# Performance work log

Hardware: AMD Instinct MI355X
Metric: run time of the kernel (lower is better)

The kernel has to match this reference:

```python
import jax, jax.numpy as jnp
import numpy as np

N_NODES = 50000
N_EDGES = 800000
IN_DIM = 128
OUT_DIM = 128
NUM_HEADS = 8
HEAD_DIM = OUT_DIM // NUM_HEADS
LN_EPS = 1e-5


def setup_inputs() -> dict:
    key = jax.random.key(0)
    ks = jax.random.split(key, 8)
    # xavier-uniform bounds
    def xavier(k, shape, fan_in, fan_out):
        a = float(np.sqrt(6.0 / (fan_in + fan_out)))
        return jax.random.uniform(k, shape, jnp.float32, -a, a)
    x = jax.random.normal(ks[0], (N_NODES, IN_DIM), jnp.float32)
    edge_index = jax.random.randint(ks[1], (2, N_EDGES), 0, N_NODES, jnp.int32)
    # store Linear weights as (in, out) so forward is x @ W (same math as torch x @ W.T)
    W_src = xavier(ks[2], (IN_DIM, OUT_DIM), IN_DIM, OUT_DIM)
    W_dst = xavier(ks[3], (IN_DIM, OUT_DIM), IN_DIM, OUT_DIM)
    attn = xavier(ks[4], (NUM_HEADS, HEAD_DIM), HEAD_DIM, NUM_HEADS)
    W_out = xavier(ks[5], (OUT_DIM, OUT_DIM), OUT_DIM, OUT_DIM)
    b_out = jnp.zeros((OUT_DIM,), jnp.float32)
    gamma = jnp.ones((OUT_DIM,), jnp.float32)
    beta = jnp.zeros((OUT_DIM,), jnp.float32)
    return {"x": x, "edge_index": edge_index, "W_src": W_src, "W_dst": W_dst,
            "attn": attn, "W_out": W_out, "b_out": b_out, "gamma": gamma, "beta": beta}


def reference(x, edge_index, W_src, W_dst, attn, W_out, b_out, gamma, beta):
    N = x.shape[0]
    H, D = attn.shape
    src, dst = edge_index[0], edge_index[1]
    # node transforms: (N, H, D)
    h_src = (x @ W_src).reshape(N, H, D)
    h_dst = (x @ W_dst).reshape(N, H, D)
    # per-edge GATv2 attention logits (E, H)
    h_src_e = h_src[src]                                  # (E, H, D)
    e = jax.nn.leaky_relu(h_src_e + h_dst[dst], 0.2)
    s = jnp.einsum('ehd,hd->eh', e, attn)
    # segment (scatter) softmax over incoming edges of each dst node
    m = jax.ops.segment_max(s, dst, num_segments=N)       # (N, H)
    exp = jnp.exp(s - m[dst])
    denom = jax.ops.segment_sum(exp, dst, num_segments=N)
    alpha = exp / (denom[dst] + 1e-8)                     # (E, H)
    # weighted message aggregation
    msg = (h_src_e * alpha[..., None]).reshape(-1, H * D)
    out = jax.ops.segment_sum(msg, dst, num_segments=N)   # (N, H*D)
    out = out @ W_out + b_out
    out = out + x                                          # residual (in_dim == out_dim)
    # LayerNorm
    mu = jnp.mean(out, axis=-1, keepdims=True)
    var = jnp.var(out, axis=-1, keepdims=True)
    out = (out - mu) * jax.lax.rsqrt(var + LN_EPS) * gamma + beta
    return out
```

## Files before the change

kernel.cpp:

```cpp
#include <hip/hip_runtime.h>
#include <hip/hip_bf16.h>

#define HEADS 8
#define CDIM 128
#define CAP 96
#define CHUNK 2048

typedef __attribute__((ext_vector_type(8))) short bf16x8;
typedef __attribute__((ext_vector_type(4))) float f32x4;

__device__ __forceinline__ unsigned short f2bs(float f) {
    union { __hip_bfloat16 b; unsigned short u; } c;
    c.b = __float2bfloat16(f);
    return c.u;
}

__device__ __forceinline__ float dpp_reduce8(float p) {
    p += __int_as_float(__builtin_amdgcn_update_dpp(0, __float_as_int(p), 0x141, 0xF, 0xF, true));
    p += __int_as_float(__builtin_amdgcn_update_dpp(0, __float_as_int(p), 0xB1,  0xF, 0xF, true));
    p += __int_as_float(__builtin_amdgcn_update_dpp(0, __float_as_int(p), 0x4E,  0xF, 0xF, true));
    return p;
}

__global__ __launch_bounds__(256) void prep_kernel(
        const int* __restrict__ ei,
        int* __restrict__ cnt,
        int* __restrict__ bucket,
        const float* __restrict__ Wsrc,
        const float* __restrict__ Wdst,
        const float* __restrict__ Wout,
        unsigned short* __restrict__ WT,
        unsigned short* __restrict__ WoT, int E, int nedgeblk) {
    const int b = blockIdx.x;
    if (b < nedgeblk) {
        const int shard = b & 7;
        const int base = (b >> 3) * CHUNK;
        int end = base + CHUNK; if (end > E) end = E;
        for (int e = base + (int)threadIdx.x; e < end; e += 256) {
            const int dst = ei[E + e];
            if ((dst & 7) == shard) {
                const int src = ei[e];
                const int pos = atomicAdd(&cnt[dst], 1);
                if (pos < CAP) bucket[(size_t)dst * CAP + pos] = src;
            }
        }
        return;
    }
    int i = (b - nedgeblk) * 256 + threadIdx.x;
    if (i < 16384)      { WT[i] = f2bs(Wsrc[(i & 127) * CDIM + (i >> 7)]); }
    else if (i < 32768) { int j = i - 16384; WT[16384 + j] = f2bs(Wdst[(j & 127) * CDIM + (j >> 7)]); }
    else if (i < 49152) { int j = i - 32768; WoT[j] = f2bs(Wout[(j & 127) * CDIM + (j >> 7)]); }
}

__global__ __launch_bounds__(256) void transform_mfma64(
        const float* __restrict__ x,
        const unsigned short* __restrict__ WT,
        unsigned short* __restrict__ hsrc,
        unsigned short* __restrict__ hdst, int N) {
    __shared__ unsigned short As[64][136];
    __shared__ unsigned short Bs[128][136];
    const int t = threadIdx.x;
    const int m0 = blockIdx.x * 64;
    const int half = blockIdx.y;
    for (int i = t; i < 64 * 32; i += 256) {
        const int r = i >> 5, kq = i & 31;
        const int gr = m0 + r;
        float4 v = make_float4(0.f, 0.f, 0.f, 0.f);
        if (gr < N) v = *(const float4*)(x + (size_t)gr * CDIM + kq * 4);
        uint2 pk;
        pk.x = (unsigned)f2bs(v.x) | ((unsigned)f2bs(v.y) << 16);
        pk.y = (unsigned)f2bs(v.z) | ((unsigned)f2bs(v.w) << 16);
        *(uint2*)&As[r][kq * 4] = pk;
    }
    const unsigned short* Wb = WT + (size_t)half * 16384;
    for (int i = t; i < 128 * 16; i += 256) {
        const int r = i >> 4, q = i & 15;
        *(uint4*)&Bs[r][q * 8] = *(const uint4*)(Wb + (size_t)r * CDIM + q * 8);
    }
    __syncthreads();
    const int w = t >> 6, lane = t & 63, l16 = lane & 15, quad = lane >> 4;
    const int wm = (w & 1) * 32, wn = (w >> 1) * 64;
    f32x4 acc[2][4];
#pragma unroll
    for (int mi = 0; mi < 2; mi++)
#pragma unroll
        for (int ni = 0; ni < 4; ni++) acc[mi][ni] = (f32x4){0.f, 0.f, 0.f, 0.f};
#pragma unroll
    for (int kc = 0; kc < 4; kc++) {
        const int k0 = kc * 32 + quad * 8;
        bf16x8 af[2], bf[4];
        af[0] = *(const bf16x8*)&As[wm + l16][k0];
        af[1] = *(const bf16x8*)&As[wm + 16 + l16][k0];
#pragma unroll
        for (int ni = 0; ni < 4; ni++)
            bf[ni] = *(const bf16x8*)&Bs[wn + ni * 16 + l16][k0];
#pragma unroll
        for (int mi = 0; mi < 2; mi++)
#pragma unroll
            for (int ni = 0; ni < 4; ni++)
                acc[mi][ni] = __builtin_amdgcn_mfma_f32_16x16x32_bf16(af[mi], bf[ni], acc[mi][ni], 0, 0, 0);
    }
    unsigned short* H = half ? hdst : hsrc;
#pragma unroll
    for (int mi = 0; mi < 2; mi++)
#pragma unroll
        for (int reg = 0; reg < 4; reg++) {
            const int gm = m0 + wm + mi * 16 + quad * 4 + reg;
            if (gm < N) {
#pragma unroll
                for (int ni = 0; ni < 4; ni++)
                    H[(size_t)gm * CDIM + wn + ni * 16 + l16] = f2bs(acc[mi][ni][reg]);
            }
        }
}

__global__ __launch_bounds__(256) void attn_agg5(
        const unsigned short* __restrict__ hsrc,
        const unsigned short* __restrict__ hdst,
        const float* __restrict__ attn,
        const int* __restrict__ cnt,
        const int* __restrict__ bucket,
        unsigned short* __restrict__ aggb) {
    __shared__ int src_lds[4][CAP];
    const int t = threadIdx.x;
    const int w = t >> 6, lane = t & 63;
    const int dst = blockIdx.x * 4 + w;
    int deg = cnt[dst];
    deg = deg > CAP ? CAP : deg;
    for (int j = lane; j < deg; j += 64)
        src_lds[w][j] = bucket[(size_t)dst * CAP + j];

    const unsigned hu = *(const unsigned*)(hdst + (size_t)dst * CDIM + lane * 2);
    const float hd0 = __uint_as_float(hu << 16);
    const float hd1 = __uint_as_float(hu & 0xffff0000u);
    const float2 a2 = ((const float2*)attn)[lane];
    const unsigned short* hb = hsrc + lane * 2;

    float l = 0.f, acc0 = 0.f, acc1 = 0.f;
    for (int j0 = 0; j0 < deg; j0 += 16) {
        unsigned vv[16];
#pragma unroll
        for (int p = 0; p < 16; p++) {
            const int j = j0 + p;
            vv[p] = (j < deg) ? *(const unsigned*)(hb + (size_t)src_lds[w][j] * CDIM) : 0u;
        }
#pragma unroll
        for (int p = 0; p < 16; p++) {
            const int j = j0 + p;
            if (j < deg) {
                const float v0 = __uint_as_float(vv[p] << 16);
                const float v1 = __uint_as_float(vv[p] & 0xffff0000u);
                float e0 = v0 + hd0; e0 = fmaxf(e0, 0.2f * e0);
                float e1 = v1 + hd1; e1 = fmaxf(e1, 0.2f * e1);
                const float pp = dpp_reduce8(e0 * a2.x + e1 * a2.y);
                const float wgt = __expf(pp);
                l += wgt;
                acc0 = fmaf(wgt, v0, acc0);
                acc1 = fmaf(wgt, v1, acc1);
            }
        }
    }
    const float r = 1.f / (l + 1e-8f);
    const unsigned o = (unsigned)f2bs(acc0 * r) | ((unsigned)f2bs(acc1 * r) << 16);
    *(unsigned*)(aggb + (size_t)dst * CDIM + lane * 2) = o;
}

__global__ __launch_bounds__(256) void out_mfma_ln64(
        const unsigned short* __restrict__ aggb,
        const float* __restrict__ x,
        const unsigned short* __restrict__ WoT,
        const float* __restrict__ bo,
        const float* __restrict__ gam,
        const float* __restrict__ bet,
        float* __restrict__ out, int N) {
    __shared__ unsigned short As[64][136];
    __shared__ unsigned short Bs[128][136];
    __shared__ float red1[64][2], red2[64][2];
    __shared__ float s_mu[64], s_rs[64];
    const int t = threadIdx.x;
    const int m0 = blockIdx.x * 64;
    for (int i = t; i < 64 * 16; i += 256) {
        const int r = i >> 4, q = i & 15;
        const int gr = m0 + r;
        uint4 v = make_uint4(0u, 0u, 0u, 0u);
        if (gr < N) v = *(const uint4*)(aggb + (size_t)gr * CDIM + q * 8);
        *(uint4*)&As[r][q * 8] = v;
    }
    for (int i = t; i < 128 * 16; i += 256) {
        const int r = i >> 4, q = i & 15;
        *(uint4*)&Bs[r][q * 8] = *(const uint4*)(WoT + (size_t)r * CDIM + q * 8);
    }
    __syncthreads();
    const int w = t >> 6, lane = t & 63, l16 = lane & 15, quad = lane >> 4;
    const int wm = (w & 1) * 32, wn = (w >> 1) * 64;
    f32x4 acc[2][4];
#pragma unroll
    for (int mi = 0; mi < 2; mi++)
#pragma unroll
        for (int ni = 0; ni < 4; ni++) acc[mi][ni] = (f32x4){0.f, 0.f, 0.f, 0.f};
#pragma unroll
    for (int kc = 0; kc < 4; kc++) {
        const int k0 = kc * 32 + quad * 8;
        bf16x8 af[2], bf[4];
        af[0] = *(const bf16x8*)&As[l16 + wm][k0];
        af[1] = *(const bf16x8*)&As[l16 + wm + 16][k0];
#pragma unroll
        for (int ni = 0; ni < 4; ni++)
            bf[ni] = *(const bf16x8*)&Bs[wn + ni * 16 + l16][k0];
#pragma unroll
        for (int mi = 0; mi < 2; mi++)
#pragma unroll
            for (int ni = 0; ni < 4; ni++)
                acc[mi][ni] = __builtin_amdgcn_mfma_f32_16x16x32_bf16(af[mi], bf[ni], acc[mi][ni], 0, 0, 0);
    }
    float bi[4], g4[4], be4[4];
#pragma unroll
    for (int ni = 0; ni < 4; ni++) {
        const int n = wn + ni * 16 + l16;
        bi[ni] = bo[n]; g4[ni] = gam[n]; be4[ni] = bet[n];
    }
#pragma unroll
    for (int mi = 0; mi < 2; mi++)
#pragma unroll
        for (int reg = 0; reg < 4; reg++) {
            const int gm = m0 + wm + mi * 16 + quad * 4 + reg;
#pragma unroll
            for (int ni = 0; ni < 4; ni++) {
                const float xr = (gm < N) ? x[(size_t)gm * CDIM + wn + ni * 16 + l16] : 0.f;
                acc[mi][ni][reg] += bi[ni] + xr;
            }
        }
#pragma unroll
    for (int mi = 0; mi < 2; mi++)
#pragma unroll
        for (int reg = 0; reg < 4; reg++) {
            float s1 = acc[mi][0][reg] + acc[mi][1][reg] + acc[mi][2][reg] + acc[mi][3][reg];
            float s2 = acc[mi][0][reg] * acc[mi][0][reg] + acc[mi][1][reg] * acc[mi][1][reg]
                     + acc[mi][2][reg] * acc[mi][2][reg] + acc[mi][3][reg] * acc[mi][3][reg];
            s1 += __shfl_xor(s1, 1, 16); s1 += __shfl_xor(s1, 2, 16);
            s1 += __shfl_xor(s1, 4, 16); s1 += __shfl_xor(s1, 8, 16);
            s2 += __shfl_xor(s2, 1, 16); s2 += __shfl_xor(s2, 2, 16);
            s2 += __shfl_xor(s2, 4, 16); s2 += __shfl_xor(s2, 8, 16);
            if (l16 == 0) {
                const int row = wm + mi * 16 + quad * 4 + reg;
                red1[row][w >> 1] = s1;
                red2[row][w >> 1] = s2;
            }
        }
    __syncthreads();
    if (t < 64) {
        const float s1 = red1[t][0] + red1[t][1];
        const float s2 = red2[t][0] + red2[t][1];
        const float mu = s1 * (1.f / 128.f);
        const float var = s2 * (1.f / 128.f) - mu * mu;
        s_mu[t] = mu;
        s_rs[t] = rsqrtf(var + 1e-5f);
    }
    __syncthreads();
#pragma unroll
    for (int mi = 0; mi < 2; mi++)
#pragma unroll
        for (int reg = 0; reg < 4; reg++) {
            const int row = wm + mi * 16 + quad * 4 + reg;
            const int gm = m0 + row;
            if (gm < N) {
                const float mu = s_mu[row], rs = s_rs[row];
#pragma unroll
                for (int ni = 0; ni < 4; ni++)
                    out[(size_t)gm * CDIM + wn + ni * 16 + l16] =
                        (acc[mi][ni][reg] - mu) * rs * g4[ni] + be4[ni];
            }
        }
}

extern "C" void kernel_launch(void* const* d_in, const int* in_sizes, int n_in,
                              void* d_out, int out_size, void* d_ws, size_t ws_size,
                              hipStream_t stream) {
    const float* x    = (const float*)d_in[0];
    const int*   ei   = (const int*)d_in[1];
    const float* Wsrc = (const float*)d_in[2];
    const float* Wdst = (const float*)d_in[3];
    const float* attn = (const float*)d_in[4];
    const float* Wout = (const float*)d_in[5];
    const float* bo   = (const float*)d_in[6];
    const float* gam  = (const float*)d_in[7];
    const float* bet  = (const float*)d_in[8];
    float* out = (float*)d_out;

    const int N = in_sizes[0] / CDIM;
    const int E = in_sizes[1] / 2;
    const int NX = N * CDIM;

    unsigned short* hsrc_b = (unsigned short*)d_ws;
    unsigned short* hdst_b = hsrc_b + (size_t)NX;
    unsigned short* aggb   = hdst_b + (size_t)NX;
    unsigned short* WT     = aggb + (size_t)NX;
    unsigned short* WoT    = WT + 32768;
    int* cnt    = (int*)(WoT + 16384);
    int* bucket = cnt + N;

    hipMemsetAsync(cnt, 0, (size_t)N * sizeof(int), stream);

    const int ngroups  = (E + CHUNK - 1) / CHUNK;
    const int nedgeblk = ngroups * 8;
    const int nwblk    = 49152 / 256;
    prep_kernel<<<nedgeblk + nwblk, 256, 0, stream>>>(ei, cnt, bucket, Wsrc, Wdst, Wout, WT, WoT, E, nedgeblk);
    transform_mfma64<<<dim3((N + 63) / 64, 2), 256, 0, stream>>>(x, WT, hsrc_b, hdst_b, N);
    attn_agg5<<<N / 4, 256, 0, stream>>>(hsrc_b, hdst_b, attn, cnt, bucket, aggb);
    out_mfma_ln64<<<(N + 63) / 64, 256, 0, stream>>>(aggb, x, WoT, bo, gam, bet, out, N);
}
```

Baseline: 203.3 us.

## Store node features in fp16, packed-half attention math, two edges per wave

The transform kernel now computes both the src and dst projections in one block, reusing the converted x tile, and writes them as fp16 instead of bf16. The attention kernel handles two edges per wave at once, 32 lanes each reading 4 features. It uses packed fp16 add, max and dot2 for the GATv2 logits, with attention weights prescaled by log2e so it can call exp2. The aim is fewer instructions per edge, a shorter DPP reduction and less redundant x loading. The cost is lower-precision logits in fp16, a cross-half shuffle reduction at the end, and extra lane work on padding edges.

```diff
diff --git a/kernel.cpp b/kernel.cpp
--- a/kernel.cpp
+++ b/kernel.cpp
@@ -5,9 +5,11 @@
 #define CDIM 128
 #define CAP 96
 #define CHUNK 2048
+#define LOG2E 1.44269504088896f
 
 typedef __attribute__((ext_vector_type(8))) short bf16x8;
 typedef __attribute__((ext_vector_type(4))) float f32x4;
+typedef __attribute__((ext_vector_type(2))) _Float16 h16x2;
 
 __device__ __forceinline__ unsigned short f2bs(float f) {
     union { __hip_bfloat16 b; unsigned short u; } c;
@@ -15,11 +17,10 @@
     return c.u;
 }
 
-__device__ __forceinline__ float dpp_reduce8(float p) {
-    p += __int_as_float(__builtin_amdgcn_update_dpp(0, __float_as_int(p), 0x141, 0xF, 0xF, true));
-    p += __int_as_float(__builtin_amdgcn_update_dpp(0, __float_as_int(p), 0xB1,  0xF, 0xF, true));
-    p += __int_as_float(__builtin_amdgcn_update_dpp(0, __float_as_int(p), 0x4E,  0xF, 0xF, true));
-    return p;
+__device__ __forceinline__ unsigned short f2hs(float f) {
+    union { _Float16 h; unsigned short u; } c;
+    c.h = (_Float16)f;
+    return c.u;
 }
 
 __global__ __launch_bounds__(256) void prep_kernel(
@@ -52,7 +53,7 @@
     else if (i < 49152) { int j = i - 32768; WoT[j] = f2bs(Wout[(j & 127) * CDIM + (j >> 7)]); }
 }
 
-__global__ __launch_bounds__(256) void transform_mfma64(
+__global__ __launch_bounds__(256) void transform_mfma64f(
         const float* __restrict__ x,
         const unsigned short* __restrict__ WT,
         unsigned short* __restrict__ hsrc,
@@ -61,7 +62,6 @@
     __shared__ unsigned short Bs[128][136];
     const int t = threadIdx.x;
     const int m0 = blockIdx.x * 64;
-    const int half = blockIdx.y;
     for (int i = t; i < 64 * 32; i += 256) {
         const int r = i >> 5, kq = i & 31;
         const int gr = m0 + r;
@@ -72,49 +72,53 @@
         pk.y = (unsigned)f2bs(v.z) | ((unsigned)f2bs(v.w) << 16);
         *(uint2*)&As[r][kq * 4] = pk;
     }
-    const unsigned short* Wb = WT + (size_t)half * 16384;
-    for (int i = t; i < 128 * 16; i += 256) {
-        const int r = i >> 4, q = i & 15;
-        *(uint4*)&Bs[r][q * 8] = *(const uint4*)(Wb + (size_t)r * CDIM + q * 8);
-    }
-    __syncthreads();
     const int w = t >> 6, lane = t & 63, l16 = lane & 15, quad = lane >> 4;
     const int wm = (w & 1) * 32, wn = (w >> 1) * 64;
-    f32x4 acc[2][4];
-#pragma unroll
-    for (int mi = 0; mi < 2; mi++)
-#pragma unroll
-        for (int ni = 0; ni < 4; ni++) acc[mi][ni] = (f32x4){0.f, 0.f, 0.f, 0.f};
-#pragma unroll
-    for (int kc = 0; kc < 4; kc++) {
-        const int k0 = kc * 32 + quad * 8;
-        bf16x8 af[2], bf[4];
-        af[0] = *(const bf16x8*)&As[wm + l16][k0];
-        af[1] = *(const bf16x8*)&As[wm + 16 + l16][k0];
-#pragma unroll
-        for (int ni = 0; ni < 4; ni++)
-            bf[ni] = *(const bf16x8*)&Bs[wn + ni * 16 + l16][k0];
+#pragma unroll
+    for (int half = 0; half < 2; half++) {
+        const unsigned short* Wb = WT + (size_t)half * 16384;
+        for (int i = t; i < 128 * 16; i += 256) {
+            const int r = i >> 4, q = i & 15;
+            *(uint4*)&Bs[r][q * 8] = *(const uint4*)(Wb + (size_t)r * CDIM + q * 8);
+        }
+        __syncthreads();
+        f32x4 acc[2][4];
 #pragma unroll
         for (int mi = 0; mi < 2; mi++)
 #pragma unroll
+            for (int ni = 0; ni < 4; ni++) acc[mi][ni] = (f32x4){0.f, 0.f, 0.f, 0.f};
+#pragma unroll
+        for (int kc = 0; kc < 4; kc++) {
+            const int k0 = kc * 32 + quad * 8;
+            bf16x8 af[2], bf[4];
+            af[0] = *(const bf16x8*)&As[wm + l16][k0];
+            af[1] = *(const bf16x8*)&As[wm + 16 + l16][k0];
+#pragma unroll
             for (int ni = 0; ni < 4; ni++)
-                acc[mi][ni] = __builtin_amdgcn_mfma_f32_16x16x32_bf16(af[mi], bf[ni], acc[mi][ni], 0, 0, 0);
-    }
-    unsigned short* H = half ? hdst : hsrc;
-#pragma unroll
-    for (int mi = 0; mi < 2; mi++)
-#pragma unroll
-        for (int reg = 0; reg < 4; reg++) {
-            const int gm = m0 + wm + mi * 16 + quad * 4 + reg;
-            if (gm < N) {
+                bf[ni] = *(const bf16x8*)&Bs[wn + ni * 16 + l16][k0];
+#pragma unroll
+            for (int mi = 0; mi < 2; mi++)
 #pragma unroll
                 for (int ni = 0; ni < 4; ni++)
-                    H[(size_t)gm * CDIM + wn + ni * 16 + l16] = f2bs(acc[mi][ni][reg]);
-            }
-        }
-}
-
-__global__ __launch_bounds__(256) void attn_agg5(
+                    acc[mi][ni] = __builtin_amdgcn_mfma_f32_16x16x32_bf16(af[mi], bf[ni], acc[mi][ni], 0, 0, 0);
+        }
+        unsigned short* H = half ? hdst : hsrc;
+#pragma unroll
+        for (int mi = 0; mi < 2; mi++)
+#pragma unroll
+            for (int reg = 0; reg < 4; reg++) {
+                const int gm = m0 + wm + mi * 16 + quad * 4 + reg;
+                if (gm < N) {
+#pragma unroll
+                    for (int ni = 0; ni < 4; ni++)
+                        H[(size_t)gm * CDIM + wn + ni * 16 + l16] = f2hs(acc[mi][ni][reg]);
+                }
+            }
+        __syncthreads();
+    }
+}
+
+__global__ __launch_bounds__(256) void attn_agg6(
         const unsigned short* __restrict__ hsrc,
         const unsigned short* __restrict__ hdst,
         const float* __restrict__ attn,
@@ -130,39 +134,62 @@
     for (int j = lane; j < deg; j += 64)
         src_lds[w][j] = bucket[(size_t)dst * CAP + j];
 
-    const unsigned hu = *(const unsigned*)(hdst + (size_t)dst * CDIM + lane * 2);
-    const float hd0 = __uint_as_float(hu << 16);
-    const float hd1 = __uint_as_float(hu & 0xffff0000u);
-    const float2 a2 = ((const float2*)attn)[lane];
-    const unsigned short* hb = hsrc + lane * 2;
-
-    float l = 0.f, acc0 = 0.f, acc1 = 0.f;
-    for (int j0 = 0; j0 < deg; j0 += 16) {
-        unsigned vv[16];
-#pragma unroll
-        for (int p = 0; p < 16; p++) {
-            const int j = j0 + p;
-            vv[p] = (j < deg) ? *(const unsigned*)(hb + (size_t)src_lds[w][j] * CDIM) : 0u;
-        }
-#pragma unroll
-        for (int p = 0; p < 16; p++) {
-            const int j = j0 + p;
-            if (j < deg) {
-                const float v0 = __uint_as_float(vv[p] << 16);
-                const float v1 = __uint_as_float(vv[p] & 0xffff0000u);
-                float e0 = v0 + hd0; e0 = fmaxf(e0, 0.2f * e0);
-                float e1 = v1 + hd1; e1 = fmaxf(e1, 0.2f * e1);
-                const float pp = dpp_reduce8(e0 * a2.x + e1 * a2.y);
-                const float wgt = __expf(pp);
-                l += wgt;
-                acc0 = fmaf(wgt, v0, acc0);
-                acc1 = fmaf(wgt, v1, acc1);
-            }
-        }
-    }
-    const float r = 1.f / (l + 1e-8f);
-    const unsigned o = (unsigned)f2bs(acc0 * r) | ((unsigned)f2bs(acc1 * r) << 16);
-    *(unsigned*)(aggb + (size_t)dst * CDIM + lane * 2) = o;
+    const int l32 = lane & 31;
+    const int eh = lane >> 5;
+    const uint2 hdu = *(const uint2*)(hdst + (size_t)dst * CDIM + l32 * 4);
+    const h16x2 hd01 = __builtin_bit_cast(h16x2, hdu.x);
+    const h16x2 hd23 = __builtin_bit_cast(h16x2, hdu.y);
+    const float4 a4 = ((const float4*)attn)[l32];
+    h16x2 a01, a23;
+    a01[0] = (_Float16)(a4.x * LOG2E); a01[1] = (_Float16)(a4.y * LOG2E);
+    a23[0] = (_Float16)(a4.z * LOG2E); a23[1] = (_Float16)(a4.w * LOG2E);
+    const h16x2 k02 = { (_Float16)0.2f, (_Float16)0.2f };
+
+    const unsigned short* hb = hsrc + l32 * 4;
+
+    float l = 0.f, acc0 = 0.f, acc1 = 0.f, acc2 = 0.f, acc3 = 0.f;
+    for (int j0 = 0; j0 < deg; j0 += 8) {
+        uint2 vv[4];
+#pragma unroll
+        for (int p = 0; p < 4; p++) {
+            const int j = j0 + 2 * p + eh;
+            const int sj = (j < deg) ? src_lds[w][j] : 0;
+            vv[p] = *(const uint2*)(hb + (size_t)sj * CDIM);
+        }
+#pragma unroll
+        for (int p = 0; p < 4; p++) {
+            const int j = j0 + 2 * p + eh;
+            const h16x2 v01 = __builtin_bit_cast(h16x2, vv[p].x);
+            const h16x2 v23 = __builtin_bit_cast(h16x2, vv[p].y);
+            h16x2 e01 = v01 + hd01;
+            h16x2 e23 = v23 + hd23;
+            e01 = __builtin_elementwise_max(e01, e01 * k02);
+            e23 = __builtin_elementwise_max(e23, e23 * k02);
+            float pp = __builtin_amdgcn_fdot2(e01, a01, 0.f, false);
+            pp = __builtin_amdgcn_fdot2(e23, a23, pp, false);
+            pp += __int_as_float(__builtin_amdgcn_update_dpp(0, __float_as_int(pp), 0xB1, 0xF, 0xF, true));
+            pp += __int_as_float(__builtin_amdgcn_update_dpp(0, __float_as_int(pp), 0x4E, 0xF, 0xF, true));
+            float wgt = __builtin_amdgcn_exp2f(pp);
+            wgt = (j < deg) ? wgt : 0.f;
+            l += wgt;
+            acc0 = fmaf(wgt, (float)v01[0], acc0);
+            acc1 = fmaf(wgt, (float)v01[1], acc1);
+            acc2 = fmaf(wgt, (float)v23[0], acc2);
+            acc3 = fmaf(wgt, (float)v23[1], acc3);
+        }
+    }
+    l    += __shfl_xor(l, 32);
+    acc0 += __shfl_xor(acc0, 32);
+    acc1 += __shfl_xor(acc1, 32);
+    acc2 += __shfl_xor(acc2, 32);
+    acc3 += __shfl_xor(acc3, 32);
+    if (lane < 32) {
+        const float r = 1.f / (l + 1e-8f);
+        uint2 o;
+        o.x = (unsigned)f2bs(acc0 * r) | ((unsigned)f2bs(acc1 * r) << 16);
+        o.y = (unsigned)f2bs(acc2 * r) | ((unsigned)f2bs(acc3 * r) << 16);
+        *(uint2*)(aggb + (size_t)dst * CDIM + l32 * 4) = o;
+    }
 }
 
 __global__ __launch_bounds__(256) void out_mfma_ln64(
@@ -291,21 +318,21 @@
     const int E = in_sizes[1] / 2;
     const int NX = N * CDIM;
 
-    unsigned short* hsrc_b = (unsigned short*)d_ws;
-    unsigned short* hdst_b = hsrc_b + (size_t)NX;
-    unsigned short* aggb   = hdst_b + (size_t)NX;
+    unsigned short* hsrc_h = (unsigned short*)d_ws;
+    unsigned short* hdst_h = hsrc_h + (size_t)NX;
+    unsigned short* aggb   = hdst_h + (size_t)NX;
     unsigned short* WT     = aggb + (size_t)NX;
     unsigned short* WoT    = WT + 32768;
     int* cnt    = (int*)(WoT + 16384);
     int* bucket = cnt + N;
 
-    hipMemsetAsync(cnt, 0, (size_t)N * sizeof(int), stream);
+    (void)hipMemsetAsync(cnt, 0, (size_t)N * sizeof(int), stream);
 
     const int ngroups  = (E + CHUNK - 1) / CHUNK;
     const int nedgeblk = ngroups * 8;
     const int nwblk    = 49152 / 256;
     prep_kernel<<<nedgeblk + nwblk, 256, 0, stream>>>(ei, cnt, bucket, Wsrc, Wdst, Wout, WT, WoT, E, nedgeblk);
-    transform_mfma64<<<dim3((N + 63) / 64, 2), 256, 0, stream>>>(x, WT, hsrc_b, hdst_b, N);
-    attn_agg5<<<N / 4, 256, 0, stream>>>(hsrc_b, hdst_b, attn, cnt, bucket, aggb);
+    transform_mfma64f<<<(N + 63) / 64, 256, 0, stream>>>(x, WT, hsrc_h, hdst_h, N);
+    attn_agg6<<<N / 4, 256, 0, stream>>>(hsrc_h, hdst_h, attn, cnt, bucket, aggb);
     out_mfma_ln64<<<(N + 63) / 64, 256, 0, stream>>>(aggb, x, WoT, bo, gam, bet, out, N);
 }
```

After: 202.0 us. Within noise of the previous version (-0.6%).
